# Optimization experiments

Hardware: AMD Instinct MI355X
Metric: run time of the kernel (lower is better)

Reference implementation:

```python
import jax, jax.numpy as jnp
import numpy as np
import math

B, S, E, H, DFF = 8, 1024, 1024, 16, 4096
DK = E // H
EPS = 1e-6


def _layernorm(x, alpha, bias):
    # Faithful to the torch module: uses unbiased std (ddof=1) and divides by (std + eps)
    mean = jnp.mean(x, axis=-1, keepdims=True)
    var = jnp.sum((x - mean) ** 2, axis=-1, keepdims=True) / (x.shape[-1] - 1)
    std = jnp.sqrt(var)
    return alpha * (x - mean) / (std + EPS) + bias


def setup_inputs() -> dict:
    key = jax.random.key(0)
    ks = jax.random.split(key, 16)
    sc_e = 1.0 / math.sqrt(E)
    sc_f = 1.0 / math.sqrt(DFF)
    inp = {
        "x": jax.random.normal(ks[0], (B, S, E), dtype=jnp.float32),
        "mask": jnp.ones((1, 1, S, S), dtype=jnp.int32),
        # linear weights stored as (in, out)
        "wq": jax.random.normal(ks[1], (E, E), jnp.float32) * sc_e,
        "bq": jnp.zeros((E,), jnp.float32),
        "wk": jax.random.normal(ks[2], (E, E), jnp.float32) * sc_e,
        "bk": jnp.zeros((E,), jnp.float32),
        "wv": jax.random.normal(ks[3], (E, E), jnp.float32) * sc_e,
        "bv": jnp.zeros((E,), jnp.float32),
        "wo": jax.random.normal(ks[4], (E, E), jnp.float32) * sc_e,
        "bo": jnp.zeros((E,), jnp.float32),
        "w1": jax.random.normal(ks[5], (E, DFF), jnp.float32) * sc_e,
        "b1": jnp.zeros((DFF,), jnp.float32),
        "w2": jax.random.normal(ks[6], (DFF, E), jnp.float32) * sc_f,
        "b2": jnp.zeros((E,), jnp.float32),
        "ln1_a": jnp.ones((E,), jnp.float32),
        "ln1_b": jnp.zeros((E,), jnp.float32),
        "ln2_a": jnp.ones((E,), jnp.float32),
        "ln2_b": jnp.zeros((E,), jnp.float32),
    }
    return inp


def _mha(x, mask, wq, bq, wk, bk, wv, bv, wo, bo):
    q = (x @ wq + bq).reshape(B, S, H, DK).transpose(0, 2, 1, 3)  # [B,H,S,DK]
    k = (x @ wk + bk).reshape(B, S, H, DK).transpose(0, 2, 1, 3)
    v = (x @ wv + bv).reshape(B, S, H, DK).transpose(0, 2, 1, 3)
    scores = jnp.einsum("bhqd,bhkd->bhqk", q, k) / math.sqrt(DK)  # [B,H,S,S]
    scores = jnp.where(mask == 0, jnp.float32(-1e9), scores)
    attn = jax.nn.softmax(scores, axis=-1)
    out = jnp.einsum("bhqk,bhkd->bhqd", attn, v)  # [B,H,S,DK]
    out = out.transpose(0, 2, 1, 3).reshape(B, S, E)
    return out @ wo + bo


def reference(x, mask, wq, bq, wk, bk, wv, bv, wo, bo, w1, b1, w2, b2,
              ln1_a, ln1_b, ln2_a, ln2_b):
    # Residual connection 1 (pre-norm): x + dropout(attn(norm(x))) ; dropout=0 at eval
    h1 = x + _mha(_layernorm(x, ln1_a, ln1_b), mask, wq, bq, wk, bk, wv, bv, wo, bo)
    # Residual connection 2: h1 + ffn(norm(h1))
    n2 = _layernorm(h1, ln2_a, ln2_b)
    ff = jax.nn.relu(n2 @ w1 + b1) @ w2 + b2
    return h1 + ff
```

## Files before the change

kernel.cpp:

```cpp
#include <hip/hip_runtime.h>
#include <hip/hip_bf16.h>
#include <cstdint>
#include <cstddef>

#define BB   8
#define SS   1024
#define EE   1024
#define HH   16
#define DKK  64
#define DFFN 4096
#define NROWS (BB*SS)

#define QSCALE 0.18033688011112042f

typedef __attribute__((ext_vector_type(8))) short short8;
typedef __attribute__((ext_vector_type(4))) short s16x4;
typedef __attribute__((ext_vector_type(4))) float f32x4;

__device__ __forceinline__ short f2bf(float f) {
  __hip_bfloat16 h = __float2bfloat16(f);
  return __builtin_bit_cast(short, h);
}

__device__ __forceinline__ float fexp2(float x) {
  float r;
  asm("v_exp_f32 %0, %1" : "=v"(r) : "v"(x));
  return r;
}

__device__ __forceinline__ void gload_lds16(const void* g, void* l) {
  __builtin_amdgcn_global_load_lds((const __attribute__((address_space(1))) void*)g,
                                   (__attribute__((address_space(3))) void*)l, 16, 0, 0);
}

__device__ __forceinline__ f32x4 mfma16(s16x4 a, s16x4 b, f32x4 c) {
#if __has_builtin(__builtin_amdgcn_mfma_f32_16x16x16_bf16)
  return __builtin_amdgcn_mfma_f32_16x16x16_bf16(a, b, c, 0, 0, 0);
#elif __has_builtin(__builtin_amdgcn_mfma_f32_16x16x16bf16_1k)
  return __builtin_amdgcn_mfma_f32_16x16x16bf16_1k(a, b, c, 0, 0, 0);
#else
  f32x4 d = c;
  asm("v_mfma_f32_16x16x16_bf16 %0, %1, %2, %0" : "+v"(d) : "v"(a), "v"(b));
  return d;
#endif
}

__global__ __launch_bounds__(256) void wtrans_kernel(const float* __restrict__ in,
                                                     short* __restrict__ out,
                                                     int R, int C) {
  __shared__ float tile[32][33];
  int c0 = blockIdx.x * 32, r0 = blockIdx.y * 32;
  int tx = threadIdx.x, ty = threadIdx.y;
#pragma unroll
  for (int i = 0; i < 32; i += 8)
    tile[ty + i][tx] = in[(size_t)(r0 + ty + i) * C + (c0 + tx)];
  __syncthreads();
#pragma unroll
  for (int i = 0; i < 32; i += 8)
    out[(size_t)(c0 + ty + i) * R + (r0 + tx)] = f2bf(tile[tx][ty + i]);
}

__global__ __launch_bounds__(256) void ln_kernel(const float* __restrict__ x,
                                                 const float* __restrict__ alpha,
                                                 const float* __restrict__ beta,
                                                 short* __restrict__ out) {
  __shared__ float sbuf[4];
  int row = blockIdx.x;
  int tid = threadIdx.x;
  const float* xr = x + (size_t)row * EE;
  float4 v = reinterpret_cast<const float4*>(xr)[tid];
  float s = v.x + v.y + v.z + v.w;
#pragma unroll
  for (int o = 32; o > 0; o >>= 1) s += __shfl_down(s, o);
  if ((tid & 63) == 0) sbuf[tid >> 6] = s;
  __syncthreads();
  float mean = (sbuf[0] + sbuf[1] + sbuf[2] + sbuf[3]) * (1.0f / EE);
  __syncthreads();
  float dx = v.x - mean, dy = v.y - mean, dz = v.z - mean, dw = v.w - mean;
  float sq = dx * dx + dy * dy + dz * dz + dw * dw;
#pragma unroll
  for (int o = 32; o > 0; o >>= 1) sq += __shfl_down(sq, o);
  if ((tid & 63) == 0) sbuf[tid >> 6] = sq;
  __syncthreads();
  float var = (sbuf[0] + sbuf[1] + sbuf[2] + sbuf[3]) * (1.0f / (EE - 1));
  float inv = 1.0f / (sqrtf(var) + 1e-6f);
  float4 a = reinterpret_cast<const float4*>(alpha)[tid];
  float4 b = reinterpret_cast<const float4*>(beta)[tid];
  size_t base = (size_t)row * EE + tid * 4;
  out[base + 0] = f2bf(a.x * dx * inv + b.x);
  out[base + 1] = f2bf(a.y * dy * inv + b.y);
  out[base + 2] = f2bf(a.z * dz * inv + b.z);
  out[base + 3] = f2bf(a.w * dw * inv + b.w);
}

template <int EPI>
__global__ __launch_bounds__(512, 2) void gemm256(const short* __restrict__ A,
                                                  const short* __restrict__ Bt,
                                                  const float* __restrict__ bias,
                                                  const float* __restrict__ resid,
                                                  void* __restrict__ out,
                                                  int N, int K, int NTN) {
  extern __shared__ char lds[];
  int tid = threadIdx.x, lane = tid & 63, w = tid >> 6;
  int wm = w >> 2, wn = w & 3;
  int g = lane >> 4, c = lane & 15;

  int nwg = gridDim.x, wg = blockIdx.x;
  int swg = (wg & 7) * (nwg >> 3) + (wg >> 3);
  int mt = swg / NTN, nt = swg % NTN;
  int m0 = mt * 256, n0 = nt * 256;

  int rS = tid >> 3;
  int gslot = (tid & 7) ^ ((tid >> 4) & 7);
  const short* pA = A + (size_t)(m0 + rS) * K + gslot * 8;
  const short* pB = Bt + (size_t)(n0 + rS) * K + gslot * 8;

#define STAGE_A(b, h, T)                                                                   \
  {                                                                                        \
    gload_lds16(pA + (size_t)((h)*128) * K + (size_t)(T)*64,                               \
                lds + (b)*32768 + (h)*16384 + tid * 16);                                   \
    gload_lds16(pA + (size_t)((h)*128 + 64) * K + (size_t)(T)*64,                          \
                lds + (b)*32768 + (h)*16384 + 8192 + tid * 16);                            \
  }
#define STAGE_B(b, h, T)                                                                   \
  {                                                                                        \
    gload_lds16(pB + (size_t)((h)*128) * K + (size_t)(T)*64,                               \
                lds + 65536 + (b)*32768 + (h)*16384 + tid * 16);                           \
    gload_lds16(pB + (size_t)((h)*128 + 64) * K + (size_t)(T)*64,                          \
                lds + 65536 + (b)*32768 + (h)*16384 + 8192 + tid * 16);                    \
  }
#define WAITV(NN) asm volatile("s_waitcnt vmcnt(" #NN ")" ::: "memory")

  int aoff0 = ((0 * 4 + g) ^ (c >> 1)) * 16;
  int aoff1 = ((1 * 4 + g) ^ (c >> 1)) * 16;
  char* ldsAb = lds + (wm * 128 + c) * 128;
  char* ldsBb = lds + 65536 + (wn * 64 + c) * 128;

  f32x4 acc[8][4] = {};
  short8 af[2][2], bfr[4][2];

#define READB(b)                                                                           \
  {                                                                                        \
    _Pragma("unroll") for (int nf = 0; nf < 4; ++nf) {                                     \
      bfr[nf][0] = *(const short8*)(ldsBb + (b)*32768 + nf * 2048 + aoff0);                \
      bfr[nf][1] = *(const short8*)(ldsBb + (b)*32768 + nf * 2048 + aoff1);                \
    }                                                                                      \
  }

#define PHASE(b, q, STAGEOP, ENDWAIT)                                                      \
  {                                                                                        \
    _Pragma("unroll") for (int mi = 0; mi < 2; ++mi) {                                     \
      af[mi][0] = *(const short8*)(ldsAb + (b)*32768 + ((q)*32 + mi * 16) * 128 + aoff0);  \
      af[mi][1] = *(const short8*)(ldsAb + (b)*32768 + ((q)*32 + mi * 16) * 128 + aoff1);  \
    }                                                                                      \
    STAGEOP;                                                                               \
    __builtin_amdgcn_s_barrier();                                                          \
    asm volatile("s_waitcnt lgkmcnt(0)" ::: "memory");                                     \
    __builtin_amdgcn_sched_barrier(0);                                                     \
    __builtin_amdgcn_s_setprio(1);                                                         \
    _Pragma("unroll") for (int mi = 0; mi < 2; ++mi)                                       \
      _Pragma("unroll") for (int nf = 0; nf < 4; ++nf) {                                   \
        acc[(q)*2 + mi][nf] = __builtin_amdgcn_mfma_f32_16x16x32_bf16(                     \
            af[mi][0], bfr[nf][0], acc[(q)*2 + mi][nf], 0, 0, 0);                          \
        acc[(q)*2 + mi][nf] = __builtin_amdgcn_mfma_f32_16x16x32_bf16(                     \
            af[mi][1], bfr[nf][1], acc[(q)*2 + mi][nf], 0, 0, 0);                          \
      }                                                                                    \
    __builtin_amdgcn_s_setprio(0);                                                         \
    ENDWAIT;                                                                               \
    __builtin_amdgcn_s_barrier();                                                          \
  }

  int NKT = K >> 6;

  STAGE_A(0, 0, 0); STAGE_A(0, 1, 0);
  STAGE_B(0, 0, 0); STAGE_B(0, 1, 0);
  STAGE_B(1, 0, 1); STAGE_B(1, 1, 1);
  WAITV(4);
  __builtin_amdgcn_s_barrier();

  for (int t = 0; t < NKT - 2; t += 2) {
    READB(0);
    PHASE(0, 0, STAGE_A(1, 0, t + 1), );
    PHASE(0, 1, STAGE_A(1, 1, t + 1), );
    PHASE(0, 2, STAGE_B(0, 0, t + 2), );
    PHASE(0, 3, STAGE_B(0, 1, t + 2), WAITV(4));
    READB(1);
    PHASE(1, 0, STAGE_A(0, 0, t + 2), );
    PHASE(1, 1, STAGE_A(0, 1, t + 2), );
    PHASE(1, 2, STAGE_B(1, 0, t + 3), );
    PHASE(1, 3, STAGE_B(1, 1, t + 3), WAITV(4));
  }
  {
    int t = NKT - 2;
    READB(0);
    PHASE(0, 0, STAGE_A(1, 0, t + 1), );
    PHASE(0, 1, STAGE_A(1, 1, t + 1), );
    PHASE(0, 2, , );
    PHASE(0, 3, , WAITV(0));
    READB(1);
    PHASE(1, 0, , );
    PHASE(1, 1, , );
    PHASE(1, 2, , );
    PHASE(1, 3, , );
  }

#undef STAGE_A
#undef STAGE_B
#undef READB
#undef PHASE
#undef WAITV

  int rb_ = m0 + wm * 128;
  int cb_ = n0 + wn * 64;
#pragma unroll
  for (int fm = 0; fm < 8; ++fm) {
#pragma unroll
    for (int nf = 0; nf < 4; ++nf) {
      int col = cb_ + nf * 16 + c;
      float bv = bias[col];
      if (EPI == 5) {
        int which = col >> 10;
        int inner = col & 1023;
        int h = inner >> 6, d = inner & 63;
        if (which < 2) {
          short* dst = (short*)out + (size_t)which * (8u * 1024 * 1024);
#pragma unroll
          for (int j = 0; j < 4; ++j) {
            int row = rb_ + fm * 16 + g * 4 + j;
            int b = row >> 10, s = row & 1023;
            float val = acc[fm][nf][j] + bv;
            if (which == 0) val *= QSCALE;
            dst[(((size_t)(b * HH + h)) * SS + s) * DKK + d] = f2bf(val);
          }
        } else {
          int row0 = rb_ + fm * 16 + g * 4;
          int b = row0 >> 10, s0 = row0 & 1023;
          s16x4 pkv;
#pragma unroll
          for (int j = 0; j < 4; ++j) pkv[j] = f2bf(acc[fm][nf][j] + bv);
          *(s16x4*)((short*)out + 2u * 8 * 1024 * 1024 +
                    (((size_t)(b * HH + h)) * DKK + d) * SS + s0) = pkv;
        }
      } else {
#pragma unroll
        for (int j = 0; j < 4; ++j) {
          int row = rb_ + fm * 16 + g * 4 + j;
          float val = acc[fm][nf][j] + bv;
          if (EPI == 1) {
            ((short*)out)[(size_t)row * N + col] = f2bf(val > 0.f ? val : 0.f);
          } else {
            ((float*)out)[(size_t)row * N + col] = resid[(size_t)row * N + col] + val;
          }
        }
      }
    }
  }
}

__global__ __launch_bounds__(512, 1) void gemm256x128(const short* __restrict__ A,
                                                      const short* __restrict__ Bt,
                                                      const float* __restrict__ bias,
                                                      const float* __restrict__ resid,
                                                      float* __restrict__ out,
                                                      int N, int K, int NTN) {
  extern __shared__ char lds[];
  int tid = threadIdx.x, lane = tid & 63, w = tid >> 6;
  int wm = w >> 1, wn = w & 1;
  int g = lane >> 4, c = lane & 15;

  int nwg = gridDim.x, wg = blockIdx.x;
  int swg = (wg & 7) * (nwg >> 3) + (wg >> 3);
  int mt = swg / NTN, nt = swg % NTN;
  int m0 = mt * 256, n0 = nt * 128;

  int rS = tid >> 3;
  int gslot = (tid & 7) ^ ((tid >> 4) & 7);
  const short* pA = A + (size_t)(m0 + rS) * K + gslot * 8;
  const short* pB = Bt + (size_t)(n0 + rS) * K + gslot * 8;

#define STAGE_A(b, h, T)                                                                   \
  {                                                                                        \
    gload_lds16(pA + (size_t)((h)*128) * K + (size_t)(T)*64,                               \
                lds + (b)*32768 + (h)*16384 + tid * 16);                                   \
    gload_lds16(pA + (size_t)((h)*128 + 64) * K + (size_t)(T)*64,                          \
                lds + (b)*32768 + (h)*16384 + 8192 + tid * 16);                            \
  }
#define STAGE_B(b, T)                                                                      \
  {                                                                                        \
    gload_lds16(pB + (size_t)(T)*64,            lds + 65536 + (b)*16384 + tid * 16);       \
    gload_lds16(pB + (size_t)64 * K + (size_t)(T)*64,                                      \
                lds + 65536 + (b)*16384 + 8192 + tid * 16);                                \
  }
#define WAITV(NN) asm volatile("s_waitcnt vmcnt(" #NN ")" ::: "memory")

  int aoff0 = ((0 * 4 + g) ^ (c >> 1)) * 16;
  int aoff1 = ((1 * 4 + g) ^ (c >> 1)) * 16;
  char* ldsAb = lds + (wm * 64 + c) * 128;
  char* ldsBb = lds + 65536 + (wn * 64 + c) * 128;

  f32x4 acc[4][4] = {};
  short8 af[2][2], bfr[4][2];

#define READB(b)                                                                           \
  {                                                                                        \
    _Pragma("unroll") for (int nf = 0; nf < 4; ++nf) {                                     \
      bfr[nf][0] = *(const short8*)(ldsBb + (b)*16384 + nf * 2048 + aoff0);                \
      bfr[nf][1] = *(const short8*)(ldsBb + (b)*16384 + nf * 2048 + aoff1);                \
    }                                                                                      \
  }

#define PHASE(b, q, STAGEOP, ENDWAIT)                                                      \
  {                                                                                        \
    _Pragma("unroll") for (int mi = 0; mi < 2; ++mi) {                                     \
      af[mi][0] = *(const short8*)(ldsAb + (b)*32768 + ((q)*32 + mi * 16) * 128 + aoff0);  \
      af[mi][1] = *(const short8*)(ldsAb + (b)*32768 + ((q)*32 + mi * 16) * 128 + aoff1);  \
    }                                                                                      \
    STAGEOP;                                                                               \
    __builtin_amdgcn_s_barrier();                                                          \
    asm volatile("s_waitcnt lgkmcnt(0)" ::: "memory");                                     \
    __builtin_amdgcn_sched_barrier(0);                                                     \
    __builtin_amdgcn_s_setprio(1);                                                         \
    _Pragma("unroll") for (int mi = 0; mi < 2; ++mi)                                       \
      _Pragma("unroll") for (int nf = 0; nf < 4; ++nf) {                                   \
        acc[(q)*2 + mi][nf] = __builtin_amdgcn_mfma_f32_16x16x32_bf16(                     \
            af[mi][0], bfr[nf][0], acc[(q)*2 + mi][nf], 0, 0, 0);                          \
        acc[(q)*2 + mi][nf] = __builtin_amdgcn_mfma_f32_16x16x32_bf16(                     \
            af[mi][1], bfr[nf][1], acc[(q)*2 + mi][nf], 0, 0, 0);                          \
      }                                                                                    \
    __builtin_amdgcn_s_setprio(0);                                                         \
    ENDWAIT;                                                                               \
    __builtin_amdgcn_s_barrier();                                                          \
  }

  int NKT = K >> 6;

  STAGE_A(0, 0, 0); STAGE_A(0, 1, 0);
  STAGE_B(0, 0);
  STAGE_B(1, 1);
  WAITV(2);
  __builtin_amdgcn_s_barrier();

  for (int t = 0; t < NKT - 2; t += 2) {
    READB(0);
    PHASE(0, 0, STAGE_A(1, 0, t + 1); STAGE_A(1, 1, t + 1), );
    PHASE(0, 1, STAGE_B(0, t + 2), WAITV(2));
    READB(1);
    PHASE(1, 0, STAGE_A(0, 0, t + 2); STAGE_A(0, 1, t + 2), );
    PHASE(1, 1, STAGE_B(1, t + 3), WAITV(2));
  }
  READB(0);
  PHASE(0, 0, STAGE_A(1, 0, NKT - 1); STAGE_A(1, 1, NKT - 1), );
  PHASE(0, 1, , WAITV(0));
  READB(1);
  PHASE(1, 0, , );
  PHASE(1, 1, , );

#undef STAGE_A
#undef STAGE_B
#undef READB
#undef PHASE
#undef WAITV

  int rb_ = m0 + wm * 64;
  int cb_ = n0 + wn * 64;
#pragma unroll
  for (int fm = 0; fm < 4; ++fm) {
#pragma unroll
    for (int nf = 0; nf < 4; ++nf) {
      int col = cb_ + nf * 16 + c;
      float bv = bias[col];
#pragma unroll
      for (int j = 0; j < 4; ++j) {
        int row = rb_ + fm * 16 + g * 4 + j;
        out[(size_t)row * N + col] = resid[(size_t)row * N + col] + acc[fm][nf][j] + bv;
      }
    }
  }
}

__global__ __launch_bounds__(256, 3) void attn_kernel(const short* __restrict__ q,
                                                      const short* __restrict__ k,
                                                      const short* __restrict__ vt,
                                                      short* __restrict__ out) {
  __shared__ short Ks[2][64 * 64];
  __shared__ short Vs[2][64 * 64];
  int bh = blockIdx.x, qt = blockIdx.y;
  int tid = threadIdx.x, lane = tid & 63, w = tid >> 6;
  int g = lane >> 4, c = lane & 15;
  const short* qp = q + (size_t)bh * SS * DKK;
  const short* kp = k + (size_t)bh * SS * DKK;
  const short* vp = vt + (size_t)bh * DKK * SS;

  int q0 = qt * 128 + w * 32;

  short8 qf[2][2];
#pragma unroll
  for (int qb = 0; qb < 2; ++qb)
#pragma unroll
    for (int ks = 0; ks < 2; ++ks)
      qf[qb][ks] = *(const short8*)(qp + (size_t)(q0 + qb * 16 + c) * DKK + ks * 32 + g * 8);

  f32x4 oacc[2][4];
#pragma unroll
  for (int qb = 0; qb < 2; ++qb)
#pragma unroll
    for (int nd = 0; nd < 4; ++nd)
#pragma unroll
      for (int j = 0; j < 4; ++j) oacc[qb][nd][j] = 0.f;
  float mrun[2] = {-1e30f, -1e30f}, lrun[2] = {0.f, 0.f};

  int rs = lane >> 3;
  int cs = lane & 7;
  int swz = (cs ^ rs) * 8;

  int buf = 0;
#define STAGE(B, T)                                                                  \
  {                                                                                  \
    _Pragma("unroll")                                                                \
    for (int cc = 0; cc < 2; ++cc) {                                                 \
      int chunk = w * 2 + cc;                                                        \
      int row = chunk * 8 + rs;                                                      \
      gload_lds16(kp + (size_t)((T) * 64 + row) * DKK + swz, &Ks[B][chunk * 512]);   \
      gload_lds16(vp + (size_t)row * SS + (T) * 64 + swz, &Vs[B][chunk * 512]);      \
    }                                                                                \
  }

  STAGE(0, 0);
  __syncthreads();

  for (int t = 0; t < SS / 64; ++t) {
    if (t < SS / 64 - 1) STAGE(buf ^ 1, t + 1);

    f32x4 sc[2][4];
#pragma unroll
    for (int qb = 0; qb < 2; ++qb)
#pragma unroll
      for (int nf = 0; nf < 4; ++nf)
#pragma unroll
        for (int j = 0; j < 4; ++j) sc[qb][nf][j] = 0.f;
    __builtin_amdgcn_s_setprio(1);
#pragma unroll
    for (int ks = 0; ks < 2; ++ks) {
      short8 kf[4];
#pragma unroll
      for (int nf = 0; nf < 4; ++nf) {
        int row = nf * 16 + c;
        int off = row * 64 + (((ks * 64 + g * 16) ^ ((c & 7) << 4)) >> 1);
        kf[nf] = *(const short8*)&Ks[buf][off];
      }
#pragma unroll
      for (int qb = 0; qb < 2; ++qb)
#pragma unroll
        for (int nf = 0; nf < 4; ++nf)
          sc[qb][nf] = __builtin_amdgcn_mfma_f32_16x16x32_bf16(kf[nf], qf[qb][ks], sc[qb][nf], 0, 0, 0);
    }
    __builtin_amdgcn_s_setprio(0);

    s16x4 pk[2][4];
#pragma unroll
    for (int qb = 0; qb < 2; ++qb) {
      float pm = -1e30f;
#pragma unroll
      for (int nf = 0; nf < 4; ++nf)
#pragma unroll
        for (int j = 0; j < 4; ++j) pm = fmaxf(pm, sc[qb][nf][j]);
      pm = fmaxf(pm, __shfl_xor(pm, 16));
      pm = fmaxf(pm, __shfl_xor(pm, 32));
      float mcur = mrun[qb];
      bool defer = __all(pm <= mcur + 8.0f);
      float mnew = defer ? mcur : fmaxf(mcur, pm);
      float rsum = 0.f;
#pragma unroll
      for (int nf = 0; nf < 4; ++nf) {
        float p0 = fexp2(sc[qb][nf][0] - mnew);
        float p1 = fexp2(sc[qb][nf][1] - mnew);
        float p2 = fexp2(sc[qb][nf][2] - mnew);
        float p3 = fexp2(sc[qb][nf][3] - mnew);
        rsum += (p0 + p1) + (p2 + p3);
        pk[qb][nf][0] = f2bf(p0); pk[qb][nf][1] = f2bf(p1);
        pk[qb][nf][2] = f2bf(p2); pk[qb][nf][3] = f2bf(p3);
      }
      rsum += __shfl_xor(rsum, 16);
      rsum += __shfl_xor(rsum, 32);
      if (defer) {
        lrun[qb] += rsum;
      } else {
        float corr = fexp2(mcur - mnew);
        mrun[qb] = mnew;
        lrun[qb] = lrun[qb] * corr + rsum;
        float cj[4];
#pragma unroll
        for (int j = 0; j < 4; ++j) cj[j] = __shfl(corr, (lane & 48) | (g * 4 + j));
#pragma unroll
        for (int nd = 0; nd < 4; ++nd)
#pragma unroll
          for (int j = 0; j < 4; ++j) oacc[qb][nd][j] *= cj[j];
      }
    }

    __builtin_amdgcn_s_setprio(1);
#pragma unroll
    for (int nf = 0; nf < 4; ++nf) {
      s16x4 vf[4];
#pragma unroll
      for (int nd = 0; nd < 4; ++nd) {
        int row = nd * 16 + c;
        int off = row * 64 + (((nf * 32 + g * 8) ^ ((c & 7) << 4)) >> 1);
        vf[nd] = *(const s16x4*)&Vs[buf][off];
      }
#pragma unroll
      for (int qb = 0; qb < 2; ++qb)
#pragma unroll
        for (int nd = 0; nd < 4; ++nd)
          oacc[qb][nd] = mfma16(pk[qb][nf], vf[nd], oacc[qb][nd]);
    }
    __builtin_amdgcn_s_setprio(0);
    __syncthreads();
    buf ^= 1;
  }
#undef STAGE

  int b = bh >> 4, h = bh & 15;
#pragma unroll
  for (int qb = 0; qb < 2; ++qb) {
#pragma unroll
    for (int j = 0; j < 4; ++j) {
      float linv = 1.0f / __shfl(lrun[qb], (lane & 48) | (g * 4 + j));
      int srow = q0 + qb * 16 + g * 4 + j;
#pragma unroll
      for (int nd = 0; nd < 4; ++nd)
        out[((size_t)b * SS + srow) * EE + h * DKK + nd * 16 + c] = f2bf(oacc[qb][nd][j] * linv);
    }
  }
}

extern "C" void kernel_launch(void* const* d_in, const int* in_sizes, int n_in,
                              void* d_out, int out_size, void* d_ws, size_t ws_size,
                              hipStream_t stream) {
  (void)in_sizes; (void)n_in; (void)out_size; (void)ws_size;
  const float* x   = (const float*)d_in[0];
  const float* wq  = (const float*)d_in[2];  const float* bq  = (const float*)d_in[3];
  const float* wk  = (const float*)d_in[4];  const float* bk  = (const float*)d_in[5];
  const float* wv  = (const float*)d_in[6];  const float* bv  = (const float*)d_in[7];
  const float* wo  = (const float*)d_in[8];  const float* bo  = (const float*)d_in[9];
  const float* w1  = (const float*)d_in[10]; const float* b1  = (const float*)d_in[11];
  const float* w2  = (const float*)d_in[12]; const float* b2  = (const float*)d_in[13];
  const float* l1a = (const float*)d_in[14]; const float* l1b = (const float*)d_in[15];
  const float* l2a = (const float*)d_in[16]; const float* l2b = (const float*)d_in[17];
  float* out = (float*)d_out;

  char* ws = (char*)d_ws;
  const size_t MB = 1024ull * 1024ull;
  short* wqkvT = (short*)(ws + 0 * MB);
  short* woT = (short*)(ws + 6 * MB);
  short* w1T = (short*)(ws + 8 * MB);
  short* w2T = (short*)(ws + 16 * MB);
  short* n1  = (short*)(ws + 24 * MB);
  short* qb  = (short*)(ws + 40 * MB);
  short* ff1 = (short*)(ws + 40 * MB);
  short* ao  = (short*)(ws + 88 * MB);
  float* bqkv = (float*)(ws + 100 * MB);
  float* h1  = (float*)(ws + 104 * MB);

  hipMemcpyAsync(bqkv,        bq, EE * sizeof(float), hipMemcpyDeviceToDevice, stream);
  hipMemcpyAsync(bqkv + EE,   bk, EE * sizeof(float), hipMemcpyDeviceToDevice, stream);
  hipMemcpyAsync(bqkv + 2*EE, bv, EE * sizeof(float), hipMemcpyDeviceToDevice, stream);

  dim3 tb(32, 8);
  wtrans_kernel<<<dim3(EE / 32, EE / 32), tb, 0, stream>>>(wq, wqkvT, EE, EE);
  wtrans_kernel<<<dim3(EE / 32, EE / 32), tb, 0, stream>>>(wk, wqkvT + 1024 * 1024, EE, EE);
  wtrans_kernel<<<dim3(EE / 32, EE / 32), tb, 0, stream>>>(wv, wqkvT + 2 * 1024 * 1024, EE, EE);
  wtrans_kernel<<<dim3(EE / 32, EE / 32), tb, 0, stream>>>(wo, woT, EE, EE);
  wtrans_kernel<<<dim3(DFFN / 32, EE / 32), tb, 0, stream>>>(w1, w1T, EE, DFFN);
  wtrans_kernel<<<dim3(EE / 32, DFFN / 32), tb, 0, stream>>>(w2, w2T, DFFN, EE);

  ln_kernel<<<NROWS, 256, 0, stream>>>(x, l1a, l1b, n1);

  gemm256<5><<<dim3(32 * 12), 512, 131072, stream>>>(n1, wqkvT, bqkv, nullptr, qb, 3072, EE, 12);

  attn_kernel<<<dim3(BB * HH, SS / 128), 256, 0, stream>>>(qb, qb + 8 * 1024 * 1024,
                                                           qb + 16 * 1024 * 1024, ao);

  gemm256x128<<<dim3(256), 512, 98304, stream>>>(ao, woT, bo, x, h1, EE, EE, 8);

  ln_kernel<<<NROWS, 256, 0, stream>>>(h1, l2a, l2b, n1);

  gemm256<1><<<dim3(32 * 16), 512, 131072, stream>>>(n1, w1T, b1, nullptr, ff1, DFFN, EE, 16);
  gemm256x128<<<dim3(256), 512, 98304, stream>>>(ff1, w2T, b2, h1, out, EE, DFFN, 8);
}
```

Before: 372.0 us.

## Merge weight prep into one kernel and run QKV GEMM on 256x128 tiles

Result: faster. 354.6 us (median of 2 runs) (-4.7%).

```diff
diff --git a/kernel.cpp b/kernel.cpp
--- a/kernel.cpp
+++ b/kernel.cpp
@@ -45,12 +45,38 @@
 #endif
 }
 
-__global__ __launch_bounds__(256) void wtrans_kernel(const float* __restrict__ in,
-                                                     short* __restrict__ out,
-                                                     int R, int C) {
+__global__ __launch_bounds__(256) void prep_kernel(
+    const float* __restrict__ wq, const float* __restrict__ wk,
+    const float* __restrict__ wv, const float* __restrict__ wo,
+    const float* __restrict__ w1, const float* __restrict__ w2,
+    const float* __restrict__ bq, const float* __restrict__ bk,
+    const float* __restrict__ bv,
+    short* __restrict__ wqkvT, short* __restrict__ woT,
+    short* __restrict__ w1T, short* __restrict__ w2T,
+    float* __restrict__ bqkv) {
+  int bid = blockIdx.x;
+  int tx = threadIdx.x, ty = threadIdx.y;
+  if (bid >= 12288) {
+    int t = ty * 32 + tx;
+    for (int i = t; i < EE; i += 256) {
+      bqkv[i] = bq[i];
+      bqkv[EE + i] = bk[i];
+      bqkv[2 * EE + i] = bv[i];
+    }
+    return;
+  }
+  const float* in;
+  short* out;
+  int R, C, t;
+  if (bid < 1024)      { in = wq; out = wqkvT;                 R = EE;   C = EE;   t = bid; }
+  else if (bid < 2048) { in = wk; out = wqkvT + 1024 * 1024;   R = EE;   C = EE;   t = bid - 1024; }
+  else if (bid < 3072) { in = wv; out = wqkvT + 2 * 1024 * 1024; R = EE; C = EE;   t = bid - 2048; }
+  else if (bid < 4096) { in = wo; out = woT;                   R = EE;   C = EE;   t = bid - 3072; }
+  else if (bid < 8192) { in = w1; out = w1T;                   R = EE;   C = DFFN; t = bid - 4096; }
+  else                 { in = w2; out = w2T;                   R = DFFN; C = EE;   t = bid - 8192; }
+  int ntx = C >> 5;
+  int c0 = (t % ntx) * 32, r0 = (t / ntx) * 32;
   __shared__ float tile[32][33];
-  int c0 = blockIdx.x * 32, r0 = blockIdx.y * 32;
-  int tx = threadIdx.x, ty = threadIdx.y;
 #pragma unroll
   for (int i = 0; i < 32; i += 8)
     tile[ty + i][tx] = in[(size_t)(r0 + ty + i) * C + (c0 + tx)];
@@ -218,50 +244,26 @@
     for (int nf = 0; nf < 4; ++nf) {
       int col = cb_ + nf * 16 + c;
       float bv = bias[col];
-      if (EPI == 5) {
-        int which = col >> 10;
-        int inner = col & 1023;
-        int h = inner >> 6, d = inner & 63;
-        if (which < 2) {
-          short* dst = (short*)out + (size_t)which * (8u * 1024 * 1024);
-#pragma unroll
-          for (int j = 0; j < 4; ++j) {
-            int row = rb_ + fm * 16 + g * 4 + j;
-            int b = row >> 10, s = row & 1023;
-            float val = acc[fm][nf][j] + bv;
-            if (which == 0) val *= QSCALE;
-            dst[(((size_t)(b * HH + h)) * SS + s) * DKK + d] = f2bf(val);
-          }
+#pragma unroll
+      for (int j = 0; j < 4; ++j) {
+        int row = rb_ + fm * 16 + g * 4 + j;
+        float val = acc[fm][nf][j] + bv;
+        if (EPI == 1) {
+          ((short*)out)[(size_t)row * N + col] = f2bf(val > 0.f ? val : 0.f);
         } else {
-          int row0 = rb_ + fm * 16 + g * 4;
-          int b = row0 >> 10, s0 = row0 & 1023;
-          s16x4 pkv;
-#pragma unroll
-          for (int j = 0; j < 4; ++j) pkv[j] = f2bf(acc[fm][nf][j] + bv);
-          *(s16x4*)((short*)out + 2u * 8 * 1024 * 1024 +
-                    (((size_t)(b * HH + h)) * DKK + d) * SS + s0) = pkv;
-        }
-      } else {
-#pragma unroll
-        for (int j = 0; j < 4; ++j) {
-          int row = rb_ + fm * 16 + g * 4 + j;
-          float val = acc[fm][nf][j] + bv;
-          if (EPI == 1) {
-            ((short*)out)[(size_t)row * N + col] = f2bf(val > 0.f ? val : 0.f);
-          } else {
-            ((float*)out)[(size_t)row * N + col] = resid[(size_t)row * N + col] + val;
-          }
+          ((float*)out)[(size_t)row * N + col] = resid[(size_t)row * N + col] + val;
         }
       }
     }
   }
 }
 
+template <int EPI>
 __global__ __launch_bounds__(512, 1) void gemm256x128(const short* __restrict__ A,
                                                       const short* __restrict__ Bt,
                                                       const float* __restrict__ bias,
                                                       const float* __restrict__ resid,
-                                                      float* __restrict__ out,
+                                                      void* __restrict__ out,
                                                       int N, int K, int NTN) {
   extern __shared__ char lds[];
   int tid = threadIdx.x, lane = tid & 63, w = tid >> 6;
@@ -369,10 +371,36 @@
     for (int nf = 0; nf < 4; ++nf) {
       int col = cb_ + nf * 16 + c;
       float bv = bias[col];
-#pragma unroll
-      for (int j = 0; j < 4; ++j) {
-        int row = rb_ + fm * 16 + g * 4 + j;
-        out[(size_t)row * N + col] = resid[(size_t)row * N + col] + acc[fm][nf][j] + bv;
+      if (EPI == 5) {
+        int which = col >> 10;
+        int inner = col & 1023;
+        int h = inner >> 6, d = inner & 63;
+        if (which < 2) {
+          short* dst = (short*)out + (size_t)which * (8u * 1024 * 1024);
+#pragma unroll
+          for (int j = 0; j < 4; ++j) {
+            int row = rb_ + fm * 16 + g * 4 + j;
+            int b = row >> 10, s = row & 1023;
+            float val = acc[fm][nf][j] + bv;
+            if (which == 0) val *= QSCALE;
+            dst[(((size_t)(b * HH + h)) * SS + s) * DKK + d] = f2bf(val);
+          }
+        } else {
+          int row0 = rb_ + fm * 16 + g * 4;
+          int b = row0 >> 10, s0 = row0 & 1023;
+          s16x4 pkv;
+#pragma unroll
+          for (int j = 0; j < 4; ++j) pkv[j] = f2bf(acc[fm][nf][j] + bv);
+          *(s16x4*)((short*)out + 2u * 8 * 1024 * 1024 +
+                    (((size_t)(b * HH + h)) * DKK + d) * SS + s0) = pkv;
+        }
+      } else {
+#pragma unroll
+        for (int j = 0; j < 4; ++j) {
+          int row = rb_ + fm * 16 + g * 4 + j;
+          ((float*)out)[(size_t)row * N + col] =
+              resid[(size_t)row * N + col] + acc[fm][nf][j] + bv;
+        }
       }
     }
   }
@@ -562,29 +590,21 @@
   float* bqkv = (float*)(ws + 100 * MB);
   float* h1  = (float*)(ws + 104 * MB);
 
-  hipMemcpyAsync(bqkv,        bq, EE * sizeof(float), hipMemcpyDeviceToDevice, stream);
-  hipMemcpyAsync(bqkv + EE,   bk, EE * sizeof(float), hipMemcpyDeviceToDevice, stream);
-  hipMemcpyAsync(bqkv + 2*EE, bv, EE * sizeof(float), hipMemcpyDeviceToDevice, stream);
-
   dim3 tb(32, 8);
-  wtrans_kernel<<<dim3(EE / 32, EE / 32), tb, 0, stream>>>(wq, wqkvT, EE, EE);
-  wtrans_kernel<<<dim3(EE / 32, EE / 32), tb, 0, stream>>>(wk, wqkvT + 1024 * 1024, EE, EE);
-  wtrans_kernel<<<dim3(EE / 32, EE / 32), tb, 0, stream>>>(wv, wqkvT + 2 * 1024 * 1024, EE, EE);
-  wtrans_kernel<<<dim3(EE / 32, EE / 32), tb, 0, stream>>>(wo, woT, EE, EE);
-  wtrans_kernel<<<dim3(DFFN / 32, EE / 32), tb, 0, stream>>>(w1, w1T, EE, DFFN);
-  wtrans_kernel<<<dim3(EE / 32, DFFN / 32), tb, 0, stream>>>(w2, w2T, DFFN, EE);
+  prep_kernel<<<dim3(12289), tb, 0, stream>>>(wq, wk, wv, wo, w1, w2, bq, bk, bv,
+                                              wqkvT, woT, w1T, w2T, bqkv);
 
   ln_kernel<<<NROWS, 256, 0, stream>>>(x, l1a, l1b, n1);
 
-  gemm256<5><<<dim3(32 * 12), 512, 131072, stream>>>(n1, wqkvT, bqkv, nullptr, qb, 3072, EE, 12);
+  gemm256x128<5><<<dim3(32 * 24), 512, 98304, stream>>>(n1, wqkvT, bqkv, nullptr, qb, 3072, EE, 24);
 
   attn_kernel<<<dim3(BB * HH, SS / 128), 256, 0, stream>>>(qb, qb + 8 * 1024 * 1024,
                                                            qb + 16 * 1024 * 1024, ao);
 
-  gemm256x128<<<dim3(256), 512, 98304, stream>>>(ao, woT, bo, x, h1, EE, EE, 8);
+  gemm256x128<2><<<dim3(256), 512, 98304, stream>>>(ao, woT, bo, x, h1, EE, EE, 8);
 
   ln_kernel<<<NROWS, 256, 0, stream>>>(h1, l2a, l2b, n1);
 
   gemm256<1><<<dim3(32 * 16), 512, 131072, stream>>>(n1, w1T, b1, nullptr, ff1, DFFN, EE, 16);
-  gemm256x128<<<dim3(256), 512, 98304, stream>>>(ff1, w2T, b2, h1, out, EE, DFFN, 8);
-}
+  gemm256x128<2><<<dim3(256), 512, 98304, stream>>>(ff1, w2T, b2, h1, out, EE, DFFN, 8);
+}
```
